# Kernel optimization log

Measured on AMD Instinct MI355X. Metric: run time of the kernel, lower is better.

The kernel has to match this reference:

```python
import jax, jax.numpy as jnp
import numpy as np

B, C, H, W = 4, 192, 56, 56


def setup_inputs() -> dict:
    key = jax.random.key(0)
    k1, k2, k3 = jax.random.split(key, 3)
    x = jax.random.normal(k1, (B, C, H, W), dtype=jnp.float32)
    conv_w = jax.random.normal(k2, (C, 2 * C), dtype=jnp.float32) * (1.0 / np.sqrt(2 * C))
    conv_b = jax.random.normal(k3, (C,), dtype=jnp.float32) * 0.01
    bn_gamma = jnp.ones((C,), dtype=jnp.float32)
    bn_beta = jnp.zeros((C,), dtype=jnp.float32)
    bn_mean = jnp.zeros((C,), dtype=jnp.float32)
    bn_var = jnp.ones((C,), dtype=jnp.float32)
    return {"x": x, "conv_w": conv_w, "conv_b": conv_b, "bn_gamma": bn_gamma,
            "bn_beta": bn_beta, "bn_mean": bn_mean, "bn_var": bn_var, "K": 4}


def reference(x, conv_w, conv_b, bn_gamma, bn_beta, bn_mean, bn_var, K):
    b, c, h, w = x.shape
    shifts_h = list(range(0, h, K))          # rolls along H
    shifts_w = list(range(K, w, K))          # rolls along W
    n = len(shifts_h) + len(shifts_w)
    scale = n ** (-0.5)
    # (B, n, C, H, W): all circularly shifted copies (static shift set)
    rolled = jnp.stack([jnp.roll(x, i, axis=2) for i in shifts_h] +
                       [jnp.roll(x, j, axis=3) for j in shifts_w], axis=1)
    # scores: tanh(scale * x * x_rolled), summed over channels -> (B, n, 1, H, W)
    scores = jnp.tanh(rolled * x[:, None] * scale).sum(axis=2, keepdims=True)
    weights = jax.nn.softmax(scores, axis=1)
    out = (rolled * weights).sum(axis=1)     # (B, C, H, W)
    cat = jnp.concatenate([x, out], axis=1)  # (B, 2C, H, W)
    # 1x1 conv as GEMM over channels
    y = jnp.einsum('bchw,oc->bohw', cat, conv_w) + conv_b[None, :, None, None]
    # BatchNorm2d in eval mode (running stats)
    eps = 1e-5
    inv = bn_gamma / jnp.sqrt(bn_var + eps)
    y = (y - bn_mean[None, :, None, None]) * inv[None, :, None, None] + bn_beta[None, :, None, None]
    return jax.nn.gelu(y, approximate=False)
```

## Files before the change

### kernel.cpp

```cpp
#include <hip/hip_runtime.h>
#include <hip/hip_bf16.h>
#include <math.h>

#define BB 4
#define CC 192
#define HH 56
#define WW 56
#define HWW 3136

typedef __attribute__((ext_vector_type(8))) short short8;
typedef __attribute__((ext_vector_type(4))) float f32x4;

__device__ __forceinline__ unsigned short f2b(float f) {
    __hip_bfloat16 h = __float2bfloat16(f);
    return __builtin_bit_cast(unsigned short, h);
}
__device__ __forceinline__ float b2f(unsigned short u) {
    unsigned int x = ((unsigned int)u) << 16;
    return __builtin_bit_cast(float, x);
}
__device__ __forceinline__ void fma4(float4& a, float w, const float4& x) {
    a.x += w * x.x; a.y += w * x.y; a.z += w * x.z; a.w += w * x.w;
}

__global__ __launch_bounds__(256) void k_pre(const float* __restrict__ x,
                                             float* __restrict__ xt,
                                             const float* __restrict__ cw,
                                             unsigned short* __restrict__ cwh,
                                             unsigned short* __restrict__ cwl) {
    int tid = threadIdx.x;
    if (blockIdx.x < 2352) {
        __shared__ float tile[32][33];
        int id = blockIdx.x;
        int b = id / 588, rem = id % 588;
        int by = rem / 98, bx = rem % 98;
        int tx = tid & 31, ty = tid >> 5;
        int p0 = bx * 32, c0 = by * 32;
#pragma unroll
        for (int i = 0; i < 4; i++) {
            int c = c0 + ty + 8 * i;
            tile[ty + 8 * i][tx] = x[(b * CC + c) * HWW + p0 + tx];
        }
        __syncthreads();
#pragma unroll
        for (int i = 0; i < 4; i++) {
            int p = p0 + ty + 8 * i;
            xt[(size_t)(b * HWW + p) * CC + c0 + tx] = tile[tx][ty + 8 * i];
        }
    } else {
        int i = (blockIdx.x - 2352) * 256 + tid;
        if (i < CC * 576) {
            int o = i / 576, k = i % 576;
            int ks = (k >= 384) ? (k - 192) : k;
            float v = cw[o * 384 + ks];
            unsigned short hi = f2b(v);
            cwh[i] = hi;
            cwl[i] = f2b(v - b2f(hi));
        }
    }
}

__global__ __launch_bounds__(256) void k_scores(const float* __restrict__ xt,
                                                float* __restrict__ sp) {
    __shared__ float Xs[28 * 100];
    int bid = blockIdx.x, tid = threadIdx.x;
    bool isH = bid < 896;
    int lid = isH ? bid : bid - 896;
    int half = lid & 1;
    int rp = (lid >> 1) & 1;
    int cb = lid >> 2;
    int b = cb / 56, l0 = cb % 56;
    int r0 = rp * 2;

    const float* src = xt + (size_t)(b * HWW) * CC + half * 96;
    for (int idx = tid; idx < 28 * 24; idx += 256) {
        int t2 = idx / 24, cq = idx % 24;
        int pi = (r0 + t2 / 14) + 4 * (t2 % 14);
        int pix = isH ? (pi * WW + l0) : (l0 * WW + pi);
        float4 v = *(const float4*)(src + (size_t)pix * CC + cq * 4);
        *(float4*)&Xs[t2 * 100 + cq * 4] = v;
    }
    __syncthreads();

    const float K2 = 0.38490017945975050f;
    int perCls = isH ? 105 : 91;
    int nI = 2 * perCls;
    if (tid < nI) {
        int cls = tid / perCls, p = tid % perCls;
        int a, bb;
        if (isH) {
            a = (int)((sqrtf((float)(8 * p + 1)) - 1.0f) * 0.5f);
            bb = p - (a * (a + 1)) / 2;
        } else {
            int ap = (int)((sqrtf((float)(8 * p + 1)) - 1.0f) * 0.5f);
            bb = p - (ap * (ap + 1)) / 2;
            a = ap + 1;
        }
        const float* pA = &Xs[(cls * 14 + a) * 100];
        const float* pB = &Xs[(cls * 14 + bb) * 100];
        float s0 = 0.f, s1 = 0.f, s2 = 0.f, s3 = 0.f;
#pragma unroll
        for (int q = 0; q < 24; q++) {
            float4 av = *(const float4*)(pA + q * 4);
            float4 bv = *(const float4*)(pB + q * 4);
            s0 += __builtin_amdgcn_rcpf(__expf(av.x * bv.x * K2) + 1.0f);
            s1 += __builtin_amdgcn_rcpf(__expf(av.y * bv.y * K2) + 1.0f);
            s2 += __builtin_amdgcn_rcpf(__expf(av.z * bv.z * K2) + 1.0f);
            s3 += __builtin_amdgcn_rcpf(__expf(av.w * bv.w * K2) + 1.0f);
        }
        float s = 96.0f - 2.0f * (s0 + s1 + s2 + s3);
        int r = r0 + cls;
        size_t base = (size_t)(half * BB + b) * HWW;
        if (isH) {
            int i1 = a - bb;
            int h1 = r + 4 * a, h2 = r + 4 * bb;
            sp[(base + h1 * WW + l0) * 32 + i1] = s;
            if (a != bb) sp[(base + h2 * WW + l0) * 32 + (14 - i1)] = s;
        } else {
            int d = a - bb;
            int w1 = r + 4 * a, w2 = r + 4 * bb;
            sp[(base + l0 * WW + w1) * 32 + 14 + (d - 1)] = s;
            sp[(base + l0 * WW + w2) * 32 + 14 + (13 - d)] = s;
        }
    }
}

__global__ __launch_bounds__(192) void k_acc(const float* __restrict__ xt,
                                             const float* __restrict__ sp,
                                             unsigned short* __restrict__ oHh,
                                             unsigned short* __restrict__ oHl,
                                             unsigned short* __restrict__ oWh,
                                             unsigned short* __restrict__ oWl) {
    __shared__ float Wt[14 * 56];
    int bid = blockIdx.x, tid = threadIdx.x;
    bool isH = bid < 224;
    int lid = isH ? bid : bid - 224;
    int b = lid / 56, l0 = lid % 56;

    if (tid < 56) {
        int pix = isH ? (tid * WW + l0) : (l0 * WW + tid);
        const float4* p0 = (const float4*)&sp[((size_t)(0 * BB + b) * HWW + pix) * 32];
        const float4* p1 = (const float4*)&sp[((size_t)(1 * BB + b) * HWW + pix) * 32];
        float sc[28];
#pragma unroll
        for (int j = 0; j < 7; j++) {
            float4 u = p0[j], v = p1[j];
            sc[4 * j + 0] = u.x + v.x; sc[4 * j + 1] = u.y + v.y;
            sc[4 * j + 2] = u.z + v.z; sc[4 * j + 3] = u.w + v.w;
        }
        float mx = -1e30f;
#pragma unroll
        for (int s = 0; s < 27; s++) mx = fmaxf(mx, sc[s]);
        float sum = 0.f;
#pragma unroll
        for (int s = 0; s < 27; s++) { sc[s] = __expf(sc[s] - mx); sum += sc[s]; }
        float inv = __builtin_amdgcn_rcpf(sum);
        if (isH) {
#pragma unroll
            for (int i = 0; i < 14; i++) Wt[i * 56 + tid] = sc[i] * inv;
        } else {
#pragma unroll
            for (int j = 0; j < 13; j++) Wt[j * 56 + tid] = sc[14 + j] * inv;
        }
    }
    __syncthreads();
    {
        int r = tid & 3, q = tid >> 2;
        float4 in[14];
#pragma unroll
        for (int t = 0; t < 14; t++) {
            int pix = isH ? ((r + 4 * t) * WW + l0) : (l0 * WW + (r + 4 * t));
            in[t] = *(const float4*)(xt + (size_t)(b * HWW + pix) * CC + q * 4);
        }
        float4 acc[14] = {};
        if (isH) {
#pragma unroll
            for (int i = 0; i < 14; i++)
#pragma unroll
                for (int a = 0; a < 14; a++)
                    fma4(acc[a], Wt[i * 56 + (r + 4 * a)], in[(a - i + 14) % 14]);
        } else {
#pragma unroll
            for (int j = 0; j < 13; j++)
#pragma unroll
                for (int a = 0; a < 14; a++)
                    fma4(acc[a], Wt[j * 56 + (r + 4 * a)], in[(a - j - 1 + 14) % 14]);
        }
        unsigned short* dh = isH ? oHh : oWh;
        unsigned short* dl = isH ? oHl : oWl;
#pragma unroll
        for (int a = 0; a < 14; a++) {
            int pix = isH ? ((r + 4 * a) * WW + l0) : (l0 * WW + (r + 4 * a));
            size_t o = (size_t)(b * HWW + pix) * CC + q * 4;
            ushort4 hi4, lo4;
            hi4.x = f2b(acc[a].x); lo4.x = f2b(acc[a].x - b2f(hi4.x));
            hi4.y = f2b(acc[a].y); lo4.y = f2b(acc[a].y - b2f(hi4.y));
            hi4.z = f2b(acc[a].z); lo4.z = f2b(acc[a].z - b2f(hi4.z));
            hi4.w = f2b(acc[a].w); lo4.w = f2b(acc[a].w - b2f(hi4.w));
            *(ushort4*)(dh + o) = hi4;
            *(ushort4*)(dl + o) = lo4;
        }
    }
}

__global__ __launch_bounds__(256) void k_conv(const float* __restrict__ xt,
                                              const unsigned short* __restrict__ oHh,
                                              const unsigned short* __restrict__ oHl,
                                              const unsigned short* __restrict__ oWh,
                                              const unsigned short* __restrict__ oWl,
                                              const unsigned short* __restrict__ cwh,
                                              const unsigned short* __restrict__ cwl,
                                              const float* __restrict__ cb,
                                              const float* __restrict__ gma,
                                              const float* __restrict__ bta,
                                              const float* __restrict__ mea,
                                              const float* __restrict__ var,
                                              float* __restrict__ y) {
    __shared__ unsigned short AB[4 * 64 * 72];
    unsigned short* Ah = AB;
    unsigned short* Al = AB + 64 * 72;
    unsigned short* Bh = AB + 2 * 64 * 72;
    unsigned short* Bl = AB + 3 * 64 * 72;
    int bm = blockIdx.x * 64, bn = blockIdx.y * 64;
    int tid = threadIdx.x, lane = tid & 63, wv = tid >> 6;

    f32x4 acc[4] = {{0,0,0,0},{0,0,0,0},{0,0,0,0},{0,0,0,0}};

    for (int kc9 = 0; kc9 < 9; kc9++) {
#pragma unroll
        for (int r2 = 0; r2 < 2; r2++) {
            int idx = tid + r2 * 256;
            int m = idx >> 3, kq = idx & 7;
            if (kc9 < 3) {
                const float* s = xt + (size_t)(bm + m) * CC + kc9 * 64 + kq * 8;
                float4 v0 = *(const float4*)s;
                float4 v1 = *(const float4*)(s + 4);
                float v[8] = {v0.x, v0.y, v0.z, v0.w, v1.x, v1.y, v1.z, v1.w};
                unsigned short hi[8], lo[8];
#pragma unroll
                for (int e = 0; e < 8; e++) {
                    hi[e] = f2b(v[e]);
                    lo[e] = f2b(v[e] - b2f(hi[e]));
                }
                *(short8*)&Ah[m * 72 + kq * 8] = *(short8*)hi;
                *(short8*)&Al[m * 72 + kq * 8] = *(short8*)lo;
            } else {
                const unsigned short* sh;
                const unsigned short* sl;
                int coff;
                if (kc9 < 6) { sh = oHh; sl = oHl; coff = (kc9 - 3) * 64; }
                else         { sh = oWh; sl = oWl; coff = (kc9 - 6) * 64; }
                size_t ao = (size_t)(bm + m) * CC + coff + kq * 8;
                *(short8*)&Ah[m * 72 + kq * 8] = *(const short8*)(sh + ao);
                *(short8*)&Al[m * 72 + kq * 8] = *(const short8*)(sl + ao);
            }
            size_t bo = (size_t)(bn + m) * 576 + kc9 * 64 + kq * 8;
            *(short8*)&Bh[m * 72 + kq * 8] = *(const short8*)(cwh + bo);
            *(short8*)&Bl[m * 72 + kq * 8] = *(const short8*)(cwl + bo);
        }
        __syncthreads();
        int n0 = wv * 16;
        int k8 = lane >> 4;
        int col = lane & 15;
#pragma unroll
        for (int ks = 0; ks < 64; ks += 32) {
            int koff = ks + k8 * 8;
            short8 bfh = *(const short8*)&Bh[(n0 + col) * 72 + koff];
            short8 bfl = *(const short8*)&Bl[(n0 + col) * 72 + koff];
#pragma unroll
            for (int fm = 0; fm < 4; fm++) {
                short8 afh = *(const short8*)&Ah[(fm * 16 + col) * 72 + koff];
                short8 afl = *(const short8*)&Al[(fm * 16 + col) * 72 + koff];
                acc[fm] = __builtin_amdgcn_mfma_f32_16x16x32_bf16(afh, bfh, acc[fm], 0, 0, 0);
                acc[fm] = __builtin_amdgcn_mfma_f32_16x16x32_bf16(afl, bfh, acc[fm], 0, 0, 0);
                acc[fm] = __builtin_amdgcn_mfma_f32_16x16x32_bf16(afh, bfl, acc[fm], 0, 0, 0);
            }
        }
        __syncthreads();
    }

    float* Ds = (float*)AB;
    {
        int col = lane & 15, rowq = lane >> 4;
#pragma unroll
        for (int fm = 0; fm < 4; fm++)
#pragma unroll
            for (int rg = 0; rg < 4; rg++)
                Ds[(fm * 16 + rowq * 4 + rg) * 68 + wv * 16 + col] = acc[fm][rg];
    }
    __syncthreads();
    {
        int o = tid >> 2, mq0 = tid & 3;
        int oo = bn + o;
        float bias = cb[oo];
        float inv  = gma[oo] * rsqrtf(var[oo] + 1e-5f);
        float mean = mea[oo], beta = bta[oo];
        int b = bm / HWW, p0 = bm % HWW;
#pragma unroll
        for (int g = 0; g < 4; g++) {
            int mq = mq0 + g * 4;
            float v[4];
#pragma unroll
            for (int j = 0; j < 4; j++) {
                float t = Ds[(mq * 4 + j) * 68 + o] + bias;
                t = (t - mean) * inv + beta;
                v[j] = 0.5f * t * (1.0f + erff(t * 0.70710678118654752f));
            }
            float4 st; st.x = v[0]; st.y = v[1]; st.z = v[2]; st.w = v[3];
            *(float4*)&y[(size_t)(b * CC + oo) * HWW + p0 + mq * 4] = st;
        }
    }
}

extern "C" void kernel_launch(void* const* d_in, const int* in_sizes, int n_in,
                              void* d_out, int out_size, void* d_ws, size_t ws_size,
                              hipStream_t stream) {
    const float* x   = (const float*)d_in[0];
    const float* cw  = (const float*)d_in[1];
    const float* cb  = (const float*)d_in[2];
    const float* gma = (const float*)d_in[3];
    const float* bta = (const float*)d_in[4];
    const float* mea = (const float*)d_in[5];
    const float* var = (const float*)d_in[6];
    float* out = (float*)d_out;

    float* ws = (float*)d_ws;
    float*          xt  = ws;
    float*          sp  = ws + 2408448;
    unsigned short* oHh = (unsigned short*)(ws + 3211264);
    unsigned short* oHl = (unsigned short*)(ws + 4415488);
    unsigned short* oWh = (unsigned short*)(ws + 5619712);
    unsigned short* oWl = (unsigned short*)(ws + 6823936);
    unsigned short* cwh = (unsigned short*)(ws + 8028160);
    unsigned short* cwl = (unsigned short*)(ws + 8083456);

    k_pre<<<2784, 256, 0, stream>>>(x, xt, cw, cwh, cwl);
    k_scores<<<1792, 256, 0, stream>>>(xt, sp);
    k_acc<<<448, 192, 0, stream>>>(xt, sp, oHh, oHl, oWh, oWl);
    k_conv<<<dim3(196, 3), 256, 0, stream>>>(xt, oHh, oHl, oWh, oWl,
                                             cwh, cwl, cb, gma, bta, mea, var, out);
}
```

Before: 132.2 us.

## Fuse four kernels into one persistent kernel with software grid barriers

Merges the transpose/weight-split, score, softmax-accumulate and MFMA conv kernels into a single persistent kernel of 448 blocks. Work is distributed with grid-stride loops, and stages are separated by atomic-counter grid barriers. The goal is to remove launch overhead and the inter-kernel gaps. In exchange, the conv stage gets less parallelism (588 tiles over 448 blocks, some doing two) and the barriers spin. The barriers also assume all 448 blocks are co-resident, which is not guaranteed.

Result: slower. 392.5 us (+196.9%).

```diff
diff --git a/kernel.cpp b/kernel.cpp
--- a/kernel.cpp
+++ b/kernel.cpp
@@ -7,6 +7,7 @@
 #define HH 56
 #define WW 56
 #define HWW 3136
+#define NBLK 448
 
 typedef __attribute__((ext_vector_type(8))) short short8;
 typedef __attribute__((ext_vector_type(4))) float f32x4;
@@ -23,33 +24,61 @@
     a.x += w * x.x; a.y += w * x.y; a.z += w * x.z; a.w += w * x.w;
 }
 
-__global__ __launch_bounds__(256) void k_pre(const float* __restrict__ x,
-                                             float* __restrict__ xt,
-                                             const float* __restrict__ cw,
-                                             unsigned short* __restrict__ cwh,
-                                             unsigned short* __restrict__ cwl) {
+__device__ __forceinline__ void gridbar(unsigned* cnt, unsigned* flag) {
+    __threadfence();
+    __syncthreads();
+    if (threadIdx.x == 0) {
+        unsigned old = atomicAdd(cnt, 1u);
+        if (old == NBLK - 1u) {
+            __threadfence();
+            atomicExch(flag, 1u);
+        } else {
+            while (atomicAdd(flag, 0u) == 0u) __builtin_amdgcn_s_sleep(4);
+            __threadfence();
+        }
+    }
+    __syncthreads();
+}
+
+__global__ void k_init(unsigned* bar) {
+    if (threadIdx.x < 8) bar[threadIdx.x] = 0u;
+}
+
+__global__ __launch_bounds__(256, 2) void k_mega(
+        const float* __restrict__ x, const float* __restrict__ cw,
+        const float* __restrict__ cb, const float* __restrict__ gma,
+        const float* __restrict__ bta, const float* __restrict__ mea,
+        const float* __restrict__ var, float* __restrict__ y,
+        float* __restrict__ xt, float* __restrict__ sp,
+        unsigned short* __restrict__ oHh, unsigned short* __restrict__ oHl,
+        unsigned short* __restrict__ oWh, unsigned short* __restrict__ oWl,
+        unsigned short* __restrict__ cwh, unsigned short* __restrict__ cwl,
+        unsigned* __restrict__ bar) {
+    __shared__ __align__(16) char smem[36864];
     int tid = threadIdx.x;
-    if (blockIdx.x < 2352) {
-        __shared__ float tile[32][33];
-        int id = blockIdx.x;
-        int b = id / 588, rem = id % 588;
-        int by = rem / 98, bx = rem % 98;
+    int bid0 = blockIdx.x;
+
+    {
+        float (*tile)[33] = (float (*)[33])smem;
         int tx = tid & 31, ty = tid >> 5;
-        int p0 = bx * 32, c0 = by * 32;
-#pragma unroll
-        for (int i = 0; i < 4; i++) {
-            int c = c0 + ty + 8 * i;
-            tile[ty + 8 * i][tx] = x[(b * CC + c) * HWW + p0 + tx];
-        }
-        __syncthreads();
-#pragma unroll
-        for (int i = 0; i < 4; i++) {
-            int p = p0 + ty + 8 * i;
-            xt[(size_t)(b * HWW + p) * CC + c0 + tx] = tile[tx][ty + 8 * i];
-        }
-    } else {
-        int i = (blockIdx.x - 2352) * 256 + tid;
-        if (i < CC * 576) {
+        for (int id = bid0; id < 2352; id += NBLK) {
+            int b = id / 588, rem = id % 588;
+            int by = rem / 98, bx = rem % 98;
+            int p0 = bx * 32, c0 = by * 32;
+            __syncthreads();
+#pragma unroll
+            for (int i = 0; i < 4; i++) {
+                int c = c0 + ty + 8 * i;
+                tile[ty + 8 * i][tx] = x[(b * CC + c) * HWW + p0 + tx];
+            }
+            __syncthreads();
+#pragma unroll
+            for (int i = 0; i < 4; i++) {
+                int p = p0 + ty + 8 * i;
+                xt[(size_t)(b * HWW + p) * CC + c0 + tx] = tile[tx][ty + 8 * i];
+            }
+        }
+        for (int i = bid0 * 256 + tid; i < CC * 576; i += NBLK * 256) {
             int o = i / 576, k = i % 576;
             int ks = (k >= 384) ? (k - 192) : k;
             float v = cw[o * 384 + ks];
@@ -58,256 +87,243 @@
             cwl[i] = f2b(v - b2f(hi));
         }
     }
-}
-
-__global__ __launch_bounds__(256) void k_scores(const float* __restrict__ xt,
-                                                float* __restrict__ sp) {
-    __shared__ float Xs[28 * 100];
-    int bid = blockIdx.x, tid = threadIdx.x;
-    bool isH = bid < 896;
-    int lid = isH ? bid : bid - 896;
-    int half = lid & 1;
-    int rp = (lid >> 1) & 1;
-    int cb = lid >> 2;
-    int b = cb / 56, l0 = cb % 56;
-    int r0 = rp * 2;
-
-    const float* src = xt + (size_t)(b * HWW) * CC + half * 96;
-    for (int idx = tid; idx < 28 * 24; idx += 256) {
-        int t2 = idx / 24, cq = idx % 24;
-        int pi = (r0 + t2 / 14) + 4 * (t2 % 14);
-        int pix = isH ? (pi * WW + l0) : (l0 * WW + pi);
-        float4 v = *(const float4*)(src + (size_t)pix * CC + cq * 4);
-        *(float4*)&Xs[t2 * 100 + cq * 4] = v;
-    }
-    __syncthreads();
-
-    const float K2 = 0.38490017945975050f;
-    int perCls = isH ? 105 : 91;
-    int nI = 2 * perCls;
-    if (tid < nI) {
-        int cls = tid / perCls, p = tid % perCls;
-        int a, bb;
-        if (isH) {
-            a = (int)((sqrtf((float)(8 * p + 1)) - 1.0f) * 0.5f);
-            bb = p - (a * (a + 1)) / 2;
-        } else {
-            int ap = (int)((sqrtf((float)(8 * p + 1)) - 1.0f) * 0.5f);
-            bb = p - (ap * (ap + 1)) / 2;
-            a = ap + 1;
-        }
-        const float* pA = &Xs[(cls * 14 + a) * 100];
-        const float* pB = &Xs[(cls * 14 + bb) * 100];
-        float s0 = 0.f, s1 = 0.f, s2 = 0.f, s3 = 0.f;
-#pragma unroll
-        for (int q = 0; q < 24; q++) {
-            float4 av = *(const float4*)(pA + q * 4);
-            float4 bv = *(const float4*)(pB + q * 4);
-            s0 += __builtin_amdgcn_rcpf(__expf(av.x * bv.x * K2) + 1.0f);
-            s1 += __builtin_amdgcn_rcpf(__expf(av.y * bv.y * K2) + 1.0f);
-            s2 += __builtin_amdgcn_rcpf(__expf(av.z * bv.z * K2) + 1.0f);
-            s3 += __builtin_amdgcn_rcpf(__expf(av.w * bv.w * K2) + 1.0f);
-        }
-        float s = 96.0f - 2.0f * (s0 + s1 + s2 + s3);
-        int r = r0 + cls;
-        size_t base = (size_t)(half * BB + b) * HWW;
-        if (isH) {
-            int i1 = a - bb;
-            int h1 = r + 4 * a, h2 = r + 4 * bb;
-            sp[(base + h1 * WW + l0) * 32 + i1] = s;
-            if (a != bb) sp[(base + h2 * WW + l0) * 32 + (14 - i1)] = s;
-        } else {
-            int d = a - bb;
-            int w1 = r + 4 * a, w2 = r + 4 * bb;
-            sp[(base + l0 * WW + w1) * 32 + 14 + (d - 1)] = s;
-            sp[(base + l0 * WW + w2) * 32 + 14 + (13 - d)] = s;
-        }
-    }
-}
-
-__global__ __launch_bounds__(192) void k_acc(const float* __restrict__ xt,
-                                             const float* __restrict__ sp,
-                                             unsigned short* __restrict__ oHh,
-                                             unsigned short* __restrict__ oHl,
-                                             unsigned short* __restrict__ oWh,
-                                             unsigned short* __restrict__ oWl) {
-    __shared__ float Wt[14 * 56];
-    int bid = blockIdx.x, tid = threadIdx.x;
-    bool isH = bid < 224;
-    int lid = isH ? bid : bid - 224;
-    int b = lid / 56, l0 = lid % 56;
-
-    if (tid < 56) {
-        int pix = isH ? (tid * WW + l0) : (l0 * WW + tid);
-        const float4* p0 = (const float4*)&sp[((size_t)(0 * BB + b) * HWW + pix) * 32];
-        const float4* p1 = (const float4*)&sp[((size_t)(1 * BB + b) * HWW + pix) * 32];
-        float sc[28];
-#pragma unroll
-        for (int j = 0; j < 7; j++) {
-            float4 u = p0[j], v = p1[j];
-            sc[4 * j + 0] = u.x + v.x; sc[4 * j + 1] = u.y + v.y;
-            sc[4 * j + 2] = u.z + v.z; sc[4 * j + 3] = u.w + v.w;
-        }
-        float mx = -1e30f;
-#pragma unroll
-        for (int s = 0; s < 27; s++) mx = fmaxf(mx, sc[s]);
-        float sum = 0.f;
-#pragma unroll
-        for (int s = 0; s < 27; s++) { sc[s] = __expf(sc[s] - mx); sum += sc[s]; }
-        float inv = __builtin_amdgcn_rcpf(sum);
-        if (isH) {
-#pragma unroll
-            for (int i = 0; i < 14; i++) Wt[i * 56 + tid] = sc[i] * inv;
-        } else {
-#pragma unroll
-            for (int j = 0; j < 13; j++) Wt[j * 56 + tid] = sc[14 + j] * inv;
-        }
-    }
-    __syncthreads();
+    gridbar(&bar[0], &bar[1]);
+
     {
-        int r = tid & 3, q = tid >> 2;
-        float4 in[14];
-#pragma unroll
-        for (int t = 0; t < 14; t++) {
-            int pix = isH ? ((r + 4 * t) * WW + l0) : (l0 * WW + (r + 4 * t));
-            in[t] = *(const float4*)(xt + (size_t)(b * HWW + pix) * CC + q * 4);
-        }
-        float4 acc[14] = {};
-        if (isH) {
-#pragma unroll
-            for (int i = 0; i < 14; i++)
-#pragma unroll
-                for (int a = 0; a < 14; a++)
-                    fma4(acc[a], Wt[i * 56 + (r + 4 * a)], in[(a - i + 14) % 14]);
-        } else {
-#pragma unroll
-            for (int j = 0; j < 13; j++)
-#pragma unroll
-                for (int a = 0; a < 14; a++)
-                    fma4(acc[a], Wt[j * 56 + (r + 4 * a)], in[(a - j - 1 + 14) % 14]);
-        }
-        unsigned short* dh = isH ? oHh : oWh;
-        unsigned short* dl = isH ? oHl : oWl;
-#pragma unroll
-        for (int a = 0; a < 14; a++) {
-            int pix = isH ? ((r + 4 * a) * WW + l0) : (l0 * WW + (r + 4 * a));
-            size_t o = (size_t)(b * HWW + pix) * CC + q * 4;
-            ushort4 hi4, lo4;
-            hi4.x = f2b(acc[a].x); lo4.x = f2b(acc[a].x - b2f(hi4.x));
-            hi4.y = f2b(acc[a].y); lo4.y = f2b(acc[a].y - b2f(hi4.y));
-            hi4.z = f2b(acc[a].z); lo4.z = f2b(acc[a].z - b2f(hi4.z));
-            hi4.w = f2b(acc[a].w); lo4.w = f2b(acc[a].w - b2f(hi4.w));
-            *(ushort4*)(dh + o) = hi4;
-            *(ushort4*)(dl + o) = lo4;
-        }
-    }
-}
-
-__global__ __launch_bounds__(256) void k_conv(const float* __restrict__ xt,
-                                              const unsigned short* __restrict__ oHh,
-                                              const unsigned short* __restrict__ oHl,
-                                              const unsigned short* __restrict__ oWh,
-                                              const unsigned short* __restrict__ oWl,
-                                              const unsigned short* __restrict__ cwh,
-                                              const unsigned short* __restrict__ cwl,
-                                              const float* __restrict__ cb,
-                                              const float* __restrict__ gma,
-                                              const float* __restrict__ bta,
-                                              const float* __restrict__ mea,
-                                              const float* __restrict__ var,
-                                              float* __restrict__ y) {
-    __shared__ unsigned short AB[4 * 64 * 72];
-    unsigned short* Ah = AB;
-    unsigned short* Al = AB + 64 * 72;
-    unsigned short* Bh = AB + 2 * 64 * 72;
-    unsigned short* Bl = AB + 3 * 64 * 72;
-    int bm = blockIdx.x * 64, bn = blockIdx.y * 64;
-    int tid = threadIdx.x, lane = tid & 63, wv = tid >> 6;
-
-    f32x4 acc[4] = {{0,0,0,0},{0,0,0,0},{0,0,0,0},{0,0,0,0}};
-
-    for (int kc9 = 0; kc9 < 9; kc9++) {
-#pragma unroll
-        for (int r2 = 0; r2 < 2; r2++) {
-            int idx = tid + r2 * 256;
-            int m = idx >> 3, kq = idx & 7;
-            if (kc9 < 3) {
-                const float* s = xt + (size_t)(bm + m) * CC + kc9 * 64 + kq * 8;
-                float4 v0 = *(const float4*)s;
-                float4 v1 = *(const float4*)(s + 4);
-                float v[8] = {v0.x, v0.y, v0.z, v0.w, v1.x, v1.y, v1.z, v1.w};
-                unsigned short hi[8], lo[8];
-#pragma unroll
-                for (int e = 0; e < 8; e++) {
-                    hi[e] = f2b(v[e]);
-                    lo[e] = f2b(v[e] - b2f(hi[e]));
-                }
-                *(short8*)&Ah[m * 72 + kq * 8] = *(short8*)hi;
-                *(short8*)&Al[m * 72 + kq * 8] = *(short8*)lo;
+        float* Xs = (float*)smem;
+        const float K2 = 0.38490017945975050f;
+#pragma unroll 1
+        for (int it = 0; it < 4; it++) {
+            int vb = bid0 + NBLK * it;
+            bool isH = vb < 896;
+            int lid = isH ? vb : vb - 896;
+            int half = lid & 1;
+            int rp = (lid >> 1) & 1;
+            int cb2 = lid >> 2;
+            int b = cb2 / 56, l0 = cb2 % 56;
+            int r0 = rp * 2;
+
+            const float* src = xt + (size_t)(b * HWW) * CC + half * 96;
+            __syncthreads();
+            for (int idx = tid; idx < 28 * 24; idx += 256) {
+                int t2 = idx / 24, cq = idx % 24;
+                int pi = (r0 + t2 / 14) + 4 * (t2 % 14);
+                int pix = isH ? (pi * WW + l0) : (l0 * WW + pi);
+                float4 v = *(const float4*)(src + (size_t)pix * CC + cq * 4);
+                *(float4*)&Xs[t2 * 100 + cq * 4] = v;
+            }
+            __syncthreads();
+
+            int perCls = isH ? 105 : 91;
+            if (tid < 2 * perCls) {
+                int cls = tid / perCls, p = tid % perCls;
+                int a, bb;
+                if (isH) {
+                    a = (int)((sqrtf((float)(8 * p + 1)) - 1.0f) * 0.5f);
+                    bb = p - (a * (a + 1)) / 2;
+                } else {
+                    int ap = (int)((sqrtf((float)(8 * p + 1)) - 1.0f) * 0.5f);
+                    bb = p - (ap * (ap + 1)) / 2;
+                    a = ap + 1;
+                }
+                const float* pA = &Xs[(cls * 14 + a) * 100];
+                const float* pB = &Xs[(cls * 14 + bb) * 100];
+                float s0 = 0.f, s1 = 0.f, s2 = 0.f, s3 = 0.f;
+#pragma unroll
+                for (int q = 0; q < 24; q++) {
+                    float4 av = *(const float4*)(pA + q * 4);
+                    float4 bv = *(const float4*)(pB + q * 4);
+                    s0 += __builtin_amdgcn_rcpf(__expf(av.x * bv.x * K2) + 1.0f);
+                    s1 += __builtin_amdgcn_rcpf(__expf(av.y * bv.y * K2) + 1.0f);
+                    s2 += __builtin_amdgcn_rcpf(__expf(av.z * bv.z * K2) + 1.0f);
+                    s3 += __builtin_amdgcn_rcpf(__expf(av.w * bv.w * K2) + 1.0f);
+                }
+                float s = 96.0f - 2.0f * (s0 + s1 + s2 + s3);
+                int r = r0 + cls;
+                size_t base = (size_t)(half * BB + b) * HWW;
+                if (isH) {
+                    int i1 = a - bb;
+                    int h1 = r + 4 * a, h2 = r + 4 * bb;
+                    sp[(base + h1 * WW + l0) * 32 + i1] = s;
+                    if (a != bb) sp[(base + h2 * WW + l0) * 32 + (14 - i1)] = s;
+                } else {
+                    int d = a - bb;
+                    int w1 = r + 4 * a, w2 = r + 4 * bb;
+                    sp[(base + l0 * WW + w1) * 32 + 14 + (d - 1)] = s;
+                    sp[(base + l0 * WW + w2) * 32 + 14 + (13 - d)] = s;
+                }
+            }
+        }
+    }
+    gridbar(&bar[2], &bar[3]);
+
+    {
+        float* Wt = (float*)smem;
+        bool isH = bid0 < 224;
+        int lid = isH ? bid0 : bid0 - 224;
+        int b = lid / 56, l0 = lid % 56;
+
+        if (tid < 56) {
+            int pix = isH ? (tid * WW + l0) : (l0 * WW + tid);
+            const float4* p0 = (const float4*)&sp[((size_t)(0 * BB + b) * HWW + pix) * 32];
+            const float4* p1 = (const float4*)&sp[((size_t)(1 * BB + b) * HWW + pix) * 32];
+            float sc[28];
+#pragma unroll
+            for (int j = 0; j < 7; j++) {
+                float4 u = p0[j], v = p1[j];
+                sc[4 * j + 0] = u.x + v.x; sc[4 * j + 1] = u.y + v.y;
+                sc[4 * j + 2] = u.z + v.z; sc[4 * j + 3] = u.w + v.w;
+            }
+            float mx = -1e30f;
+#pragma unroll
+            for (int s = 0; s < 27; s++) mx = fmaxf(mx, sc[s]);
+            float sum = 0.f;
+#pragma unroll
+            for (int s = 0; s < 27; s++) { sc[s] = __expf(sc[s] - mx); sum += sc[s]; }
+            float inv = __builtin_amdgcn_rcpf(sum);
+            if (isH) {
+#pragma unroll
+                for (int i = 0; i < 14; i++) Wt[i * 56 + tid] = sc[i] * inv;
             } else {
-                const unsigned short* sh;
-                const unsigned short* sl;
-                int coff;
-                if (kc9 < 6) { sh = oHh; sl = oHl; coff = (kc9 - 3) * 64; }
-                else         { sh = oWh; sl = oWl; coff = (kc9 - 6) * 64; }
-                size_t ao = (size_t)(bm + m) * CC + coff + kq * 8;
-                *(short8*)&Ah[m * 72 + kq * 8] = *(const short8*)(sh + ao);
-                *(short8*)&Al[m * 72 + kq * 8] = *(const short8*)(sl + ao);
-            }
-            size_t bo = (size_t)(bn + m) * 576 + kc9 * 64 + kq * 8;
-            *(short8*)&Bh[m * 72 + kq * 8] = *(const short8*)(cwh + bo);
-            *(short8*)&Bl[m * 72 + kq * 8] = *(const short8*)(cwl + bo);
+#pragma unroll
+                for (int j = 0; j < 13; j++) Wt[j * 56 + tid] = sc[14 + j] * inv;
+            }
         }
         __syncthreads();
-        int n0 = wv * 16;
-        int k8 = lane >> 4;
-        int col = lane & 15;
-#pragma unroll
-        for (int ks = 0; ks < 64; ks += 32) {
-            int koff = ks + k8 * 8;
-            short8 bfh = *(const short8*)&Bh[(n0 + col) * 72 + koff];
-            short8 bfl = *(const short8*)&Bl[(n0 + col) * 72 + koff];
-#pragma unroll
-            for (int fm = 0; fm < 4; fm++) {
-                short8 afh = *(const short8*)&Ah[(fm * 16 + col) * 72 + koff];
-                short8 afl = *(const short8*)&Al[(fm * 16 + col) * 72 + koff];
-                acc[fm] = __builtin_amdgcn_mfma_f32_16x16x32_bf16(afh, bfh, acc[fm], 0, 0, 0);
-                acc[fm] = __builtin_amdgcn_mfma_f32_16x16x32_bf16(afl, bfh, acc[fm], 0, 0, 0);
-                acc[fm] = __builtin_amdgcn_mfma_f32_16x16x32_bf16(afh, bfl, acc[fm], 0, 0, 0);
-            }
-        }
-        __syncthreads();
-    }
-
-    float* Ds = (float*)AB;
+        if (tid < 192) {
+            int r = tid & 3, q = tid >> 2;
+            float4 in[14];
+#pragma unroll
+            for (int t = 0; t < 14; t++) {
+                int pix = isH ? ((r + 4 * t) * WW + l0) : (l0 * WW + (r + 4 * t));
+                in[t] = *(const float4*)(xt + (size_t)(b * HWW + pix) * CC + q * 4);
+            }
+            float4 acc[14] = {};
+            if (isH) {
+#pragma unroll
+                for (int i = 0; i < 14; i++)
+#pragma unroll
+                    for (int a = 0; a < 14; a++)
+                        fma4(acc[a], Wt[i * 56 + (r + 4 * a)], in[(a - i + 14) % 14]);
+            } else {
+#pragma unroll
+                for (int j = 0; j < 13; j++)
+#pragma unroll
+                    for (int a = 0; a < 14; a++)
+                        fma4(acc[a], Wt[j * 56 + (r + 4 * a)], in[(a - j - 1 + 14) % 14]);
+            }
+            unsigned short* dh = isH ? oHh : oWh;
+            unsigned short* dl = isH ? oHl : oWl;
+#pragma unroll
+            for (int a = 0; a < 14; a++) {
+                int pix = isH ? ((r + 4 * a) * WW + l0) : (l0 * WW + (r + 4 * a));
+                size_t o = (size_t)(b * HWW + pix) * CC + q * 4;
+                ushort4 hi4, lo4;
+                hi4.x = f2b(acc[a].x); lo4.x = f2b(acc[a].x - b2f(hi4.x));
+                hi4.y = f2b(acc[a].y); lo4.y = f2b(acc[a].y - b2f(hi4.y));
+                hi4.z = f2b(acc[a].z); lo4.z = f2b(acc[a].z - b2f(hi4.z));
+                hi4.w = f2b(acc[a].w); lo4.w = f2b(acc[a].w - b2f(hi4.w));
+                *(ushort4*)(dh + o) = hi4;
+                *(ushort4*)(dl + o) = lo4;
+            }
+        }
+    }
+    gridbar(&bar[4], &bar[5]);
+
     {
-        int col = lane & 15, rowq = lane >> 4;
-#pragma unroll
-        for (int fm = 0; fm < 4; fm++)
-#pragma unroll
-            for (int rg = 0; rg < 4; rg++)
-                Ds[(fm * 16 + rowq * 4 + rg) * 68 + wv * 16 + col] = acc[fm][rg];
-    }
-    __syncthreads();
-    {
-        int o = tid >> 2, mq0 = tid & 3;
-        int oo = bn + o;
-        float bias = cb[oo];
-        float inv  = gma[oo] * rsqrtf(var[oo] + 1e-5f);
-        float mean = mea[oo], beta = bta[oo];
-        int b = bm / HWW, p0 = bm % HWW;
-#pragma unroll
-        for (int g = 0; g < 4; g++) {
-            int mq = mq0 + g * 4;
-            float v[4];
-#pragma unroll
-            for (int j = 0; j < 4; j++) {
-                float t = Ds[(mq * 4 + j) * 68 + o] + bias;
-                t = (t - mean) * inv + beta;
-                v[j] = 0.5f * t * (1.0f + erff(t * 0.70710678118654752f));
-            }
-            float4 st; st.x = v[0]; st.y = v[1]; st.z = v[2]; st.w = v[3];
-            *(float4*)&y[(size_t)(b * CC + oo) * HWW + p0 + mq * 4] = st;
+        unsigned short* Ah = (unsigned short*)smem;
+        unsigned short* Al = Ah + 64 * 72;
+        unsigned short* Bh = Ah + 2 * 64 * 72;
+        unsigned short* Bl = Ah + 3 * 64 * 72;
+        float* Ds = (float*)smem;
+        int lane = tid & 63, wv = tid >> 6;
+#pragma unroll 1
+        for (int v = bid0; v < 588; v += NBLK) {
+            int bm = (v % 196) * 64, bn = (v / 196) * 64;
+            __syncthreads();
+            f32x4 acc[4] = {{0,0,0,0},{0,0,0,0},{0,0,0,0},{0,0,0,0}};
+            for (int kc9 = 0; kc9 < 9; kc9++) {
+#pragma unroll
+                for (int r2 = 0; r2 < 2; r2++) {
+                    int idx = tid + r2 * 256;
+                    int m = idx >> 3, kq = idx & 7;
+                    if (kc9 < 3) {
+                        const float* s = xt + (size_t)(bm + m) * CC + kc9 * 64 + kq * 8;
+                        float4 v0 = *(const float4*)s;
+                        float4 v1 = *(const float4*)(s + 4);
+                        float vv[8] = {v0.x, v0.y, v0.z, v0.w, v1.x, v1.y, v1.z, v1.w};
+                        unsigned short hi[8], lo[8];
+#pragma unroll
+                        for (int e = 0; e < 8; e++) {
+                            hi[e] = f2b(vv[e]);
+                            lo[e] = f2b(vv[e] - b2f(hi[e]));
+                        }
+                        *(short8*)&Ah[m * 72 + kq * 8] = *(short8*)hi;
+                        *(short8*)&Al[m * 72 + kq * 8] = *(short8*)lo;
+                    } else {
+                        const unsigned short* sh;
+                        const unsigned short* sl;
+                        int coff;
+                        if (kc9 < 6) { sh = oHh; sl = oHl; coff = (kc9 - 3) * 64; }
+                        else         { sh = oWh; sl = oWl; coff = (kc9 - 6) * 64; }
+                        size_t ao = (size_t)(bm + m) * CC + coff + kq * 8;
+                        *(short8*)&Ah[m * 72 + kq * 8] = *(const short8*)(sh + ao);
+                        *(short8*)&Al[m * 72 + kq * 8] = *(const short8*)(sl + ao);
+                    }
+                    size_t bo = (size_t)(bn + m) * 576 + kc9 * 64 + kq * 8;
+                    *(short8*)&Bh[m * 72 + kq * 8] = *(const short8*)(cwh + bo);
+                    *(short8*)&Bl[m * 72 + kq * 8] = *(const short8*)(cwl + bo);
+                }
+                __syncthreads();
+                int n0 = wv * 16;
+                int k8 = lane >> 4;
+                int col = lane & 15;
+#pragma unroll
+                for (int ks = 0; ks < 64; ks += 32) {
+                    int koff = ks + k8 * 8;
+                    short8 bfh = *(const short8*)&Bh[(n0 + col) * 72 + koff];
+                    short8 bfl = *(const short8*)&Bl[(n0 + col) * 72 + koff];
+#pragma unroll
+                    for (int fm = 0; fm < 4; fm++) {
+                        short8 afh = *(const short8*)&Ah[(fm * 16 + col) * 72 + koff];
+                        short8 afl = *(const short8*)&Al[(fm * 16 + col) * 72 + koff];
+                        acc[fm] = __builtin_amdgcn_mfma_f32_16x16x32_bf16(afh, bfh, acc[fm], 0, 0, 0);
+                        acc[fm] = __builtin_amdgcn_mfma_f32_16x16x32_bf16(afl, bfh, acc[fm], 0, 0, 0);
+                        acc[fm] = __builtin_amdgcn_mfma_f32_16x16x32_bf16(afh, bfl, acc[fm], 0, 0, 0);
+                    }
+                }
+                __syncthreads();
+            }
+            {
+                int col = lane & 15, rowq = lane >> 4;
+#pragma unroll
+                for (int fm = 0; fm < 4; fm++)
+#pragma unroll
+                    for (int rg = 0; rg < 4; rg++)
+                        Ds[(fm * 16 + rowq * 4 + rg) * 68 + wv * 16 + col] = acc[fm][rg];
+            }
+            __syncthreads();
+            {
+                int o = tid >> 2, mq0 = tid & 3;
+                int oo = bn + o;
+                float bias = cb[oo];
+                float inv  = gma[oo] * rsqrtf(var[oo] + 1e-5f);
+                float mean = mea[oo], beta = bta[oo];
+                int b = bm / HWW, p0 = bm % HWW;
+#pragma unroll
+                for (int g = 0; g < 4; g++) {
+                    int mq = mq0 + g * 4;
+                    float vv[4];
+#pragma unroll
+                    for (int j = 0; j < 4; j++) {
+                        float t = Ds[(mq * 4 + j) * 68 + o] + bias;
+                        t = (t - mean) * inv + beta;
+                        vv[j] = 0.5f * t * (1.0f + erff(t * 0.70710678118654752f));
+                    }
+                    float4 st; st.x = vv[0]; st.y = vv[1]; st.z = vv[2]; st.w = vv[3];
+                    *(float4*)&y[(size_t)(b * CC + oo) * HWW + p0 + mq * 4] = st;
+                }
+            }
         }
     }
 }
@@ -333,10 +349,9 @@
     unsigned short* oWl = (unsigned short*)(ws + 6823936);
     unsigned short* cwh = (unsigned short*)(ws + 8028160);
     unsigned short* cwl = (unsigned short*)(ws + 8083456);
-
-    k_pre<<<2784, 256, 0, stream>>>(x, xt, cw, cwh, cwl);
-    k_scores<<<1792, 256, 0, stream>>>(xt, sp);
-    k_acc<<<448, 192, 0, stream>>>(xt, sp, oHh, oHl, oWh, oWl);
-    k_conv<<<dim3(196, 3), 256, 0, stream>>>(xt, oHh, oHl, oWh, oWl,
-                                             cwh, cwl, cb, gma, bta, mea, var, out);
-}
+    unsigned*       bar = (unsigned*)(ws + 8138752);
+
+    k_init<<<1, 64, 0, stream>>>(bar);
+    k_mega<<<NBLK, 256, 0, stream>>>(x, cw, cb, gma, bta, mea, var, out,
+                                     xt, sp, oHh, oHl, oWh, oWl, cwh, cwl, bar);
+}
```
